# Kernel optimization log

Measured on AMD Instinct MI355X. Metric: run time of the kernel, lower is better.

Reference implementation:

```python
import jax, jax.numpy as jnp
import numpy as np

N_NODES = 100000
N_EDGES = 1600000
DIM = 128
K_LAYERS = 3


def setup_inputs() -> dict:
    key = jax.random.key(0)
    ks = jax.random.split(key, 6)
    x = jax.random.normal(ks[0], (N_NODES, DIM), dtype=jnp.float32)
    edge_index = jax.random.randint(ks[1], (2, N_EDGES), 0, N_NODES, dtype=jnp.int64)
    scale = 1.0 / np.sqrt(DIM)
    W1 = jax.random.normal(ks[2], (K_LAYERS, DIM, DIM), dtype=jnp.float32) * scale
    b1 = jnp.zeros((K_LAYERS, DIM), dtype=jnp.float32)
    W2 = jax.random.normal(ks[3], (K_LAYERS, DIM, DIM), dtype=jnp.float32) * scale
    b2 = jnp.zeros((K_LAYERS, DIM), dtype=jnp.float32)
    return {"x": x, "edge_index": edge_index, "W1": W1, "b1": b1, "W2": W2, "b2": b2}


def reference(x, edge_index, W1, b1, W2, b2):
    # GINConv (PyG, eps=0): out = MLP(x + sum_{j -> i} x_j)
    src = edge_index[0]  # message source nodes (x_j)
    dst = edge_index[1]  # aggregation targets
    n = x.shape[0]
    for i in range(K_LAYERS):
        agg = jax.ops.segment_sum(x[src], dst, num_segments=n)  # [N, D]
        h = x + agg                                             # (1+eps)*x + agg, eps=0
        h = jax.nn.relu(h @ W1[i] + b1[i])
        x = h @ W2[i] + b2[i]
    return x
```

## Files before the change

### kernel.cpp

```cpp
#include <hip/hip_runtime.h>
#include <hip/hip_bf16.h>
#include <cstddef>

#define DIM_C 128
typedef unsigned short ushort_t;
typedef unsigned int uint_t;

constexpr int TILE_N = 64;
constexpr int BLOCK  = 256;
constexpr int HP2    = DIM_C + 8;
constexpr int CAP    = 64;

typedef __attribute__((ext_vector_type(8))) short bf16x8;
typedef __attribute__((ext_vector_type(4))) float f32x4;

__device__ inline ushort_t f2bf(float x) {
    __hip_bfloat16 h = __float2bfloat16(x);
    return *reinterpret_cast<ushort_t*>(&h);
}

__global__ void cvt_bf16(const float* __restrict__ src, ushort_t* __restrict__ dst, int n8) {
    int i = blockIdx.x * blockDim.x + threadIdx.x;
    if (i < n8) {
        float4 a = ((const float4*)src)[2 * i];
        float4 b = ((const float4*)src)[2 * i + 1];
        union { ushort_t us[8]; uint4 u; } pk;
        pk.us[0] = f2bf(a.x); pk.us[1] = f2bf(a.y); pk.us[2] = f2bf(a.z); pk.us[3] = f2bf(a.w);
        pk.us[4] = f2bf(b.x); pk.us[5] = f2bf(b.y); pk.us[6] = f2bf(b.z); pk.us[7] = f2bf(b.w);
        ((uint4*)dst)[i] = pk.u;
    }
}

__global__ void cvt_wt(const float* __restrict__ W1, const float* __restrict__ W2,
                       ushort_t* __restrict__ Wt1, ushort_t* __restrict__ Wt2, int per) {
    int idx = blockIdx.x * blockDim.x + threadIdx.x;
    if (idx < 2 * per) {
        const float* src = (idx < per) ? W1 : W2;
        ushort_t* dst    = (idx < per) ? Wt1 : Wt2;
        int r = (idx < per) ? idx : idx - per;
        int l = r >> 14, rr = r & 16383, n = rr >> 7, k = rr & 127;
        dst[r] = f2bf(src[(l << 14) + (k << 7) + n]);
    }
}

__global__ void bucket_fill(const int* __restrict__ srcv, const int* __restrict__ dstv, int E,
                            int* __restrict__ cnt, int* __restrict__ col) {
    int e4 = blockIdx.x * blockDim.x + threadIdx.x;
    int e = e4 * 4;
    if (e + 4 <= E) {
        int4 d = ((const int4*)dstv)[e4];
        int4 s = ((const int4*)srcv)[e4];
        int p;
        p = atomicAdd(&cnt[d.x], 1); if (p < CAP) col[(size_t)d.x * CAP + p] = s.x;
        p = atomicAdd(&cnt[d.y], 1); if (p < CAP) col[(size_t)d.y * CAP + p] = s.y;
        p = atomicAdd(&cnt[d.z], 1); if (p < CAP) col[(size_t)d.z * CAP + p] = s.z;
        p = atomicAdd(&cnt[d.w], 1); if (p < CAP) col[(size_t)d.w * CAP + p] = s.w;
    } else {
        for (; e < E; ++e) {
            int d = dstv[e];
            int p = atomicAdd(&cnt[d], 1);
            if (p < CAP) col[(size_t)d * CAP + p] = srcv[e];
        }
    }
}

__device__ inline void acc_bf8(float* acc, uint4 v) {
    uint_t w[4] = {v.x, v.y, v.z, v.w};
    #pragma unroll
    for (int k = 0; k < 4; ++k) {
        acc[2 * k]     += __uint_as_float(w[k] << 16);
        acc[2 * k + 1] += __uint_as_float(w[k] & 0xffff0000u);
    }
}

template <int U>
__device__ inline void gq(float* acc, const ushort_t* __restrict__ xb,
                          int cc, int qb, int j, int lq) {
    int cs[U];
    #pragma unroll
    for (int u = 0; u < U; ++u) cs[u] = __shfl(cc, qb + j + u);
    uint4 v[U];
    #pragma unroll
    for (int u = 0; u < U; ++u)
        v[u] = ((const uint4*)(xb + (size_t)cs[u] * DIM_C))[lq];
    #pragma unroll
    for (int u = 0; u < U; ++u) acc_bf8(acc, v[u]);
}

__global__ __launch_bounds__(BLOCK, 4)
void gin_layer(const ushort_t* __restrict__ xb,
               const int* __restrict__ cnt,
               const int* __restrict__ col,
               const ushort_t* __restrict__ Wt1, const float* __restrict__ b1,
               const ushort_t* __restrict__ Wt2, const float* __restrict__ b2,
               float* __restrict__ xout_f, ushort_t* __restrict__ xout_b,
               int n_nodes)
{
    __shared__ __align__(16) ushort_t hb16[TILE_N * HP2];

    const int tid  = threadIdx.x;
    const int wave = tid >> 6;
    const int lane = tid & 63;
    const int q    = lane >> 4;
    const int lq   = lane & 15;
    const int qb   = 16 * q;
    const int node0 = blockIdx.x * TILE_N;
    const int w16   = wave * 16;

    {
        int cl = 0;
        if (lane < 16) {
            int nd = node0 + w16 + lane;
            cl = (nd < n_nodes) ? cnt[nd] : 0;
        }

        int n0s = min(node0 + w16 + q, n_nodes - 1);
        int c0 = col[(size_t)n0s * CAP + lq];
        int c1 = col[(size_t)n0s * CAP + 16 + lq];

        for (int i = 0; i < 4; ++i) {
            const int ln = w16 + i * 4 + q;
            const int n  = node0 + ln;
            const int nsafe = min(n, n_nodes - 1);
            const int cq = min(__shfl(cl, i * 4 + q), CAP);

            int cn0 = 0, cn1 = 0;
            if (i < 3) {
                int n1s = min(node0 + w16 + (i + 1) * 4 + q, n_nodes - 1);
                cn0 = col[(size_t)n1s * CAP + lq];
                cn1 = col[(size_t)n1s * CAP + 16 + lq];
            }

            float acc[8] = {0.f, 0.f, 0.f, 0.f, 0.f, 0.f, 0.f, 0.f};
            if (n < n_nodes) {
                uint4 sv = ((const uint4*)(xb + (size_t)n * DIM_C))[lq];
                acc_bf8(acc, sv);
            }

            for (int blk = 0; blk < 4; ++blk) {
                int mq = cq - blk * 16;
                mq = max(0, min(mq, 16));
                if (!__any(mq > 0)) break;
                int cc = (blk == 0) ? c0 : (blk == 1) ? c1
                         : col[(size_t)nsafe * CAP + blk * 16 + lq];
                if (mq == 16) {
                    gq<16>(acc, xb, cc, qb, 0, lq);
                } else {
                    int j = 0;
                    if (j + 8 <= mq) { gq<8>(acc, xb, cc, qb, j, lq); j += 8; }
                    if (j + 4 <= mq) { gq<4>(acc, xb, cc, qb, j, lq); j += 4; }
                    if (j + 2 <= mq) { gq<2>(acc, xb, cc, qb, j, lq); j += 2; }
                    if (j < mq)      { gq<1>(acc, xb, cc, qb, j, lq); }
                }
            }

            union { ushort_t us[8]; uint4 u; } pk;
            #pragma unroll
            for (int k = 0; k < 8; ++k) pk.us[k] = f2bf(acc[k]);
            *(uint4*)&hb16[ln * HP2 + 8 * lq] = pk.u;

            c0 = cn0; c1 = cn1;
        }
    }

    const int ml   = lane & 15;
    const int quad = lane >> 4;

    f32x4 acc1[8];
    #pragma unroll
    for (int nn = 0; nn < 8; ++nn) {
        float bv = b1[nn * 16 + ml];
        f32x4 a; a[0] = bv; a[1] = bv; a[2] = bv; a[3] = bv;
        acc1[nn] = a;
    }
    #pragma unroll
    for (int kk = 0; kk < 4; ++kk) {
        bf16x8 af = *(const bf16x8*)&hb16[(w16 + ml) * HP2 + kk * 32 + quad * 8];
        #pragma unroll
        for (int nn = 0; nn < 8; ++nn) {
            bf16x8 bf = *(const bf16x8*)&Wt1[(size_t)(nn * 16 + ml) * DIM_C + kk * 32 + quad * 8];
            acc1[nn] = __builtin_amdgcn_mfma_f32_16x16x32_bf16(af, bf, acc1[nn], 0, 0, 0);
        }
    }
    #pragma unroll
    for (int nn = 0; nn < 8; ++nn) {
        #pragma unroll
        for (int r = 0; r < 4; ++r) {
            hb16[(w16 + quad * 4 + r) * HP2 + nn * 16 + ml] = f2bf(fmaxf(acc1[nn][r], 0.f));
        }
    }

    f32x4 acc2[8];
    #pragma unroll
    for (int nn = 0; nn < 8; ++nn) {
        float bv = b2[nn * 16 + ml];
        f32x4 a; a[0] = bv; a[1] = bv; a[2] = bv; a[3] = bv;
        acc2[nn] = a;
    }
    #pragma unroll
    for (int kk = 0; kk < 4; ++kk) {
        bf16x8 af = *(const bf16x8*)&hb16[(w16 + ml) * HP2 + kk * 32 + quad * 8];
        #pragma unroll
        for (int nn = 0; nn < 8; ++nn) {
            bf16x8 bf = *(const bf16x8*)&Wt2[(size_t)(nn * 16 + ml) * DIM_C + kk * 32 + quad * 8];
            acc2[nn] = __builtin_amdgcn_mfma_f32_16x16x32_bf16(af, bf, acc2[nn], 0, 0, 0);
        }
    }

    #pragma unroll
    for (int nn = 0; nn < 8; ++nn) {
        #pragma unroll
        for (int r = 0; r < 4; ++r) {
            const int node = node0 + w16 + quad * 4 + r;
            if (node < n_nodes) {
                if (xout_f) xout_f[(size_t)node * DIM_C + nn * 16 + ml] = acc2[nn][r];
                else        xout_b[(size_t)node * DIM_C + nn * 16 + ml] = f2bf(acc2[nn][r]);
            }
        }
    }
}

extern "C" void kernel_launch(void* const* d_in, const int* in_sizes, int n_in,
                              void* d_out, int out_size, void* d_ws, size_t ws_size,
                              hipStream_t stream) {
    const float* x  = (const float*)d_in[0];
    const int* eidx = (const int*)d_in[1];
    const float* W1 = (const float*)d_in[2];
    const float* b1 = (const float*)d_in[3];
    const float* W2 = (const float*)d_in[4];
    const float* b2 = (const float*)d_in[5];
    float* out = (float*)d_out;

    const int N = in_sizes[0] / DIM_C;
    const int E = in_sizes[1] / 2;

    ushort_t* xb0 = (ushort_t*)d_ws;
    int* cnt      = (int*)(xb0 + (size_t)N * DIM_C);
    int* col      = cnt + N;
    ushort_t* Wt1 = (ushort_t*)(col + (size_t)N * CAP);
    ushort_t* Wt2 = Wt1 + 3 * DIM_C * DIM_C;
    ushort_t* xb1 = (ushort_t*)d_out;

    const int* srcv = eidx;
    const int* dstv = eidx + E;

    cvt_bf16<<<((N * DIM_C / 8) + 255) / 256, 256, 0, stream>>>(x, xb0, N * DIM_C / 8);
    cvt_wt<<<(2 * 3 * DIM_C * DIM_C + 255) / 256, 256, 0, stream>>>(W1, W2, Wt1, Wt2, 3 * DIM_C * DIM_C);
    hipMemsetAsync(cnt, 0, (size_t)N * sizeof(int), stream);
    bucket_fill<<<((E + 3) / 4 + 255) / 256, 256, 0, stream>>>(srcv, dstv, E, cnt, col);

    const int nblk = (N + TILE_N - 1) / TILE_N;
    const int WS = DIM_C * DIM_C;
    gin_layer<<<nblk, BLOCK, 0, stream>>>(xb0, cnt, col, Wt1,          b1,       Wt2,          b2,       nullptr, xb1, N);
    gin_layer<<<nblk, BLOCK, 0, stream>>>(xb1, cnt, col, Wt1 + WS,     b1 + 128, Wt2 + WS,     b2 + 128, nullptr, xb0, N);
    gin_layer<<<nblk, BLOCK, 0, stream>>>(xb0, cnt, col, Wt1 + 2 * WS, b1 + 256, Wt2 + 2 * WS, b2 + 256, out, nullptr, N);
}
```

Baseline: 569.2 us.

## Slice edge bucketing by destination range and merge conversion kernels

```diff
diff --git a/kernel.cpp b/kernel.cpp
--- a/kernel.cpp
+++ b/kernel.cpp
@@ -13,53 +13,76 @@
 
 typedef __attribute__((ext_vector_type(8))) short bf16x8;
 typedef __attribute__((ext_vector_type(4))) float f32x4;
+typedef int intx4 __attribute__((ext_vector_type(4)));
 
 __device__ inline ushort_t f2bf(float x) {
     __hip_bfloat16 h = __float2bfloat16(x);
     return *reinterpret_cast<ushort_t*>(&h);
 }
 
-__global__ void cvt_bf16(const float* __restrict__ src, ushort_t* __restrict__ dst, int n8) {
+__global__ void cvt_all(const float* __restrict__ x, ushort_t* __restrict__ xb,
+                        const float* __restrict__ W1, const float* __restrict__ W2,
+                        ushort_t* __restrict__ Wt1, ushort_t* __restrict__ Wt2,
+                        int n8, int per) {
     int i = blockIdx.x * blockDim.x + threadIdx.x;
     if (i < n8) {
-        float4 a = ((const float4*)src)[2 * i];
-        float4 b = ((const float4*)src)[2 * i + 1];
+        float4 a = ((const float4*)x)[2 * i];
+        float4 b = ((const float4*)x)[2 * i + 1];
         union { ushort_t us[8]; uint4 u; } pk;
         pk.us[0] = f2bf(a.x); pk.us[1] = f2bf(a.y); pk.us[2] = f2bf(a.z); pk.us[3] = f2bf(a.w);
         pk.us[4] = f2bf(b.x); pk.us[5] = f2bf(b.y); pk.us[6] = f2bf(b.z); pk.us[7] = f2bf(b.w);
-        ((uint4*)dst)[i] = pk.u;
-    }
-}
-
-__global__ void cvt_wt(const float* __restrict__ W1, const float* __restrict__ W2,
-                       ushort_t* __restrict__ Wt1, ushort_t* __restrict__ Wt2, int per) {
-    int idx = blockIdx.x * blockDim.x + threadIdx.x;
-    if (idx < 2 * per) {
-        const float* src = (idx < per) ? W1 : W2;
-        ushort_t* dst    = (idx < per) ? Wt1 : Wt2;
-        int r = (idx < per) ? idx : idx - per;
-        int l = r >> 14, rr = r & 16383, n = rr >> 7, k = rr & 127;
-        dst[r] = f2bf(src[(l << 14) + (k << 7) + n]);
-    }
-}
-
-__global__ void bucket_fill(const int* __restrict__ srcv, const int* __restrict__ dstv, int E,
-                            int* __restrict__ cnt, int* __restrict__ col) {
-    int e4 = blockIdx.x * blockDim.x + threadIdx.x;
-    int e = e4 * 4;
-    if (e + 4 <= E) {
-        int4 d = ((const int4*)dstv)[e4];
-        int4 s = ((const int4*)srcv)[e4];
-        int p;
-        p = atomicAdd(&cnt[d.x], 1); if (p < CAP) col[(size_t)d.x * CAP + p] = s.x;
-        p = atomicAdd(&cnt[d.y], 1); if (p < CAP) col[(size_t)d.y * CAP + p] = s.y;
-        p = atomicAdd(&cnt[d.z], 1); if (p < CAP) col[(size_t)d.z * CAP + p] = s.z;
-        p = atomicAdd(&cnt[d.w], 1); if (p < CAP) col[(size_t)d.w * CAP + p] = s.w;
+        ((uint4*)xb)[i] = pk.u;
     } else {
-        for (; e < E; ++e) {
-            int d = dstv[e];
-            int p = atomicAdd(&cnt[d], 1);
-            if (p < CAP) col[(size_t)d * CAP + p] = srcv[e];
+        int idx = i - n8;
+        if (idx < 2 * per) {
+            const float* src = (idx < per) ? W1 : W2;
+            ushort_t* dst    = (idx < per) ? Wt1 : Wt2;
+            int r = (idx < per) ? idx : idx - per;
+            int l = r >> 14, rr = r & 16383, n = rr >> 7, k = rr & 127;
+            dst[r] = f2bf(src[(l << 14) + (k << 7) + n]);
+        }
+    }
+}
+
+constexpr int NGRP   = 8;
+constexpr int NCHUNK = 256;
+
+__global__ __launch_bounds__(256)
+void bucket_sliced(const int* __restrict__ srcv, const int* __restrict__ dstv,
+                   int E, int N, int* __restrict__ cnt, int* __restrict__ col) {
+    const int grp   = blockIdx.x & (NGRP - 1);
+    const int chunk = blockIdx.x >> 3;
+    const int RW = (N + NGRP - 1) / NGRP;
+    const int lo = grp * RW;
+    const int Q  = E >> 2;
+    const int QP = (Q + NCHUNK - 1) / NCHUNK;
+    const int q0 = chunk * QP;
+    const int q1 = min(Q, q0 + QP);
+    const intx4* d4p = (const intx4*)dstv;
+    const intx4* s4p = (const intx4*)srcv;
+
+    for (int q = q0 + threadIdx.x; q < q1; q += 256) {
+        intx4 d = __builtin_nontemporal_load(&d4p[q]);
+        const bool a0 = (unsigned)(d.x - lo) < (unsigned)RW;
+        const bool a1 = (unsigned)(d.y - lo) < (unsigned)RW;
+        const bool a2 = (unsigned)(d.z - lo) < (unsigned)RW;
+        const bool a3 = (unsigned)(d.w - lo) < (unsigned)RW;
+        if (a0 | a1 | a2 | a3) {
+            intx4 s = __builtin_nontemporal_load(&s4p[q]);
+            int p;
+            if (a0) { p = atomicAdd(&cnt[d.x], 1); if (p < CAP) col[(size_t)d.x * CAP + p] = s.x; }
+            if (a1) { p = atomicAdd(&cnt[d.y], 1); if (p < CAP) col[(size_t)d.y * CAP + p] = s.y; }
+            if (a2) { p = atomicAdd(&cnt[d.z], 1); if (p < CAP) col[(size_t)d.z * CAP + p] = s.z; }
+            if (a3) { p = atomicAdd(&cnt[d.w], 1); if (p < CAP) col[(size_t)d.w * CAP + p] = s.w; }
+        }
+    }
+    if (chunk == 0) {
+        for (int e = (Q << 2) + threadIdx.x; e < E; e += 256) {
+            int dd = dstv[e];
+            if ((unsigned)(dd - lo) < (unsigned)RW) {
+                int p = atomicAdd(&cnt[dd], 1);
+                if (p < CAP) col[(size_t)dd * CAP + p] = srcv[e];
+            }
         }
     }
 }
@@ -244,10 +267,11 @@
     const int* srcv = eidx;
     const int* dstv = eidx + E;
 
-    cvt_bf16<<<((N * DIM_C / 8) + 255) / 256, 256, 0, stream>>>(x, xb0, N * DIM_C / 8);
-    cvt_wt<<<(2 * 3 * DIM_C * DIM_C + 255) / 256, 256, 0, stream>>>(W1, W2, Wt1, Wt2, 3 * DIM_C * DIM_C);
+    const int n8  = N * DIM_C / 8;
+    const int per = 3 * DIM_C * DIM_C;
+    cvt_all<<<(n8 + 2 * per + 255) / 256, 256, 0, stream>>>(x, xb0, W1, W2, Wt1, Wt2, n8, per);
     hipMemsetAsync(cnt, 0, (size_t)N * sizeof(int), stream);
-    bucket_fill<<<((E + 3) / 4 + 255) / 256, 256, 0, stream>>>(srcv, dstv, E, cnt, col);
+    bucket_sliced<<<NGRP * NCHUNK, 256, 0, stream>>>(srcv, dstv, E, N, cnt, col);
 
     const int nblk = (N + TILE_N - 1) / TILE_N;
     const int WS = DIM_C * DIM_C;
```

Measured after the change: 515.0 us. 1.11x faster.
